# Optimization experiments

Measured on AMD Instinct MI355X. Metric: run time of the kernel, lower is better.

The kernel has to match this reference:

```python
import jax, jax.numpy as jnp
import numpy as np

B, L, D = 8, 2048, 1024
MASKED = -2.0 ** 31  # fp32 path of the torch code


def setup_inputs() -> dict:
    key = jax.random.key(0)
    ks = jax.random.split(key, 11)
    s = 1.0 / np.sqrt(D)
    return {
        "Q": jax.random.normal(ks[0], (B, L, D), jnp.float32),
        "K": jax.random.normal(ks[1], (B, L, D), jnp.float32),
        "V": jax.random.normal(ks[2], (B, L, D), jnp.float32),
        "Wq": jax.random.normal(ks[3], (D, D), jnp.float32) * s,
        "bq": jax.random.normal(ks[4], (D,), jnp.float32) * s,
        "Wk": jax.random.normal(ks[5], (D, D), jnp.float32) * s,
        "bk": jax.random.normal(ks[6], (D,), jnp.float32) * s,
        "Wv": jax.random.normal(ks[7], (D, D), jnp.float32) * s,
        "bv": jax.random.normal(ks[8], (D,), jnp.float32) * s,
        "q_mask": jax.random.randint(ks[9], (B, L), 0, 2, jnp.int32),
        "k_mask": jax.random.randint(ks[10], (B, L), 0, 2, jnp.int32),
    }


def reference(Q, K, V, Wq, bq, Wk, bk, Wv, bv, q_mask, k_mask):
    # with_projection=True: linear projections (torch Linear: x @ W.T + b)
    Qp = jnp.einsum("bld,ed->ble", Q, Wq) + bq
    Kp = jnp.einsum("bld,ed->ble", K, Wk) + bk
    Vp = jnp.einsum("bld,ed->ble", V, Wv) + bv
    # NOTE: source hard-sets scale = 1 after computing sqrt(d_hidden)
    e = jnp.einsum("bqd,bkd->bqk", Qp, Kp)            # [B, Lq, Lk]
    e = jnp.where(k_mask[:, None, :] == 0, MASKED, e)  # masked_fill on key axis
    a = jax.nn.softmax(e, axis=-1)                     # with_sparse=False
    # dropout is identity in eval/reference mode
    a = jnp.einsum("bqk,bkd->bqd", a, Vp)
    a = jnp.where(q_mask[:, :, None] == 0, 0.0, a)     # zero masked query rows
    return a, e
```

## Files before the change

### kernel.cpp

```cpp
#include <hip/hip_runtime.h>
#include <cstddef>
#include <cstdint>

constexpr int Bn = 8;
constexpr int Ln = 2048;
constexpr int Dn = 1024;
constexpr float MASKED_VAL = -2147483648.0f;

typedef unsigned short u16;
typedef unsigned int   u32;
typedef __attribute__((ext_vector_type(8))) __bf16 bf16x8;
typedef __attribute__((ext_vector_type(4))) float  f32x4;

__device__ __forceinline__ u16 f2bf(float x) {
    u32 u = __float_as_uint(x);
    u += 0x7FFFu + ((u >> 16) & 1u);
    return (u16)(u >> 16);
}
__device__ __forceinline__ float bf2f(u16 h) {
    return __uint_as_float(((u32)h) << 16);
}
__device__ __forceinline__ u32 pack2(float a, float b) {
    return (u32)f2bf(a) | ((u32)f2bf(b) << 16);
}
__device__ __forceinline__ int rup(int x, int m) { return (x + m - 1) & ~(m - 1); }

__device__ __forceinline__ void gload16(const void* g, void* l) {
    typedef const __attribute__((address_space(1))) unsigned int* gp_t;
    typedef __attribute__((address_space(3))) unsigned int* lp_t;
    __builtin_amdgcn_global_load_lds((gp_t)g, (lp_t)l, 16, 0, 0);
}

#define MFMA16(a, b, c) __builtin_amdgcn_mfma_f32_16x16x32_bf16((a), (b), (c), 0, 0, 0)

__global__ __launch_bounds__(256) void prep_kernel(
    const int* __restrict__ k_mask, const int* __restrict__ q_mask,
    int* __restrict__ kidx, int* __restrict__ kpos,
    int* __restrict__ qidx, int* __restrict__ qpos, int* __restrict__ cnts)
{
    __shared__ int sc[256];
    __shared__ int lastv;
    const int b = blockIdx.x, t = threadIdx.x;
    for (int pass = 0; pass < 2; ++pass) {
        const int* msk = (pass ? q_mask : k_mask) + b * Ln;
        int* idx = (pass ? qidx : kidx) + b * Ln;
        int* pos = (pass ? qpos : kpos) + b * Ln;
        int f[8], s = 0;
        #pragma unroll
        for (int j = 0; j < 8; ++j) { f[j] = (msk[t * 8 + j] != 0) ? 1 : 0; s += f[j]; }
        sc[t] = s;
        __syncthreads();
        #pragma unroll
        for (int o = 1; o < 256; o <<= 1) {
            int v = (t >= o) ? sc[t - o] : 0;
            __syncthreads();
            sc[t] += v;
            __syncthreads();
        }
        int incl = sc[t];
        int total = sc[255];
        int p = incl - s;
        #pragma unroll
        for (int j = 0; j < 8; ++j) {
            pos[t * 8 + j] = f[j] ? p : -1;
            if (f[j]) { idx[p] = t * 8 + j; ++p; }
        }
        __syncthreads();
        if (t == 0) {
            cnts[b * 2 + pass] = total;
            lastv = (total > 0) ? idx[total - 1] : 0;
        }
        __syncthreads();
        int padv = (pass == 0) ? lastv : 0;
        for (int e2 = total + t; e2 < Ln; e2 += 256) idx[e2] = padv;
        __syncthreads();
    }
}

__global__ __launch_bounds__(256) void convert_single_kernel(
    const float* __restrict__ src, u16* __restrict__ dh, int n)
{
    int i = (blockIdx.x * 256 + threadIdx.x) * 8;
    if (i >= n) return;
    float f[8];
    *(float4*)&f[0] = *(const float4*)(src + i);
    *(float4*)&f[4] = *(const float4*)(src + i + 4);
    u32 H[4];
    #pragma unroll
    for (int j = 0; j < 4; ++j) H[j] = pack2(f[2*j], f[2*j+1]);
    *(uint4*)(dh + i) = make_uint4(H[0], H[1], H[2], H[3]);
}

__global__ __launch_bounds__(256) void convgather_kernel(
    const float* __restrict__ K, const float* __restrict__ V,
    const int* __restrict__ kidx, const int* __restrict__ cnts,
    u16* __restrict__ Xkc, u16* __restrict__ Vc)
{
    const int b = blockIdx.z, j = blockIdx.x, y = blockIdx.y;
    if (j >= rup(cnts[b * 2], 128)) return;
    const int src_row = kidx[b * Ln + j];
    const float* src = (y ? V : K) + ((size_t)b * Ln + src_row) * Dn;
    u16* dst = (y ? Vc : Xkc) + ((size_t)b * Ln + j) * Dn;
    const int t = threadIdx.x;
    float4 f = *(const float4*)(src + t * 4);
    *(uint2*)(dst + t * 4) = make_uint2(pack2(f.x, f.y), pack2(f.z, f.w));
}

__global__ __launch_bounds__(256) void wtrans_kernel(
    const float* __restrict__ Wq, const float* __restrict__ Wk,
    u16* __restrict__ Wqt, u16* __restrict__ Wkt)
{
    __shared__ float tile[64][68];
    const float* src = blockIdx.z ? Wk : Wq;
    u16* dst = blockIdx.z ? Wkt : Wqt;
    const int e0 = blockIdx.y * 64, d0 = blockIdx.x * 64;
    const int t = threadIdx.x;
    const int r = t >> 2, cq = (t & 3) * 16;
    const float* s = src + (size_t)(e0 + r) * Dn + d0 + cq;
    #pragma unroll
    for (int i = 0; i < 4; ++i)
        *(float4*)&tile[r][cq + i * 4] = *(const float4*)(s + i * 4);
    __syncthreads();
    u32 o[8];
    #pragma unroll
    for (int i = 0; i < 8; ++i)
        o[i] = pack2(tile[cq + 2 * i][r], tile[cq + 2 * i + 1][r]);
    u16* d = dst + (size_t)(d0 + r) * Dn + e0 + cq;
    *(uint4*)(d)     = make_uint4(o[0], o[1], o[2], o[3]);
    *(uint4*)(d + 8) = make_uint4(o[4], o[5], o[6], o[7]);
}

__global__ __launch_bounds__(64) void ck_kernel(
    const float* __restrict__ bq, const float* __restrict__ bk, float* __restrict__ cbuf)
{
    int l = threadIdx.x;
    float s = 0.f;
    #pragma unroll
    for (int i = 0; i < 16; ++i) s += bq[l + 64 * i] * bk[l + 64 * i];
    #pragma unroll
    for (int o = 32; o; o >>= 1) s += __shfl_xor(s, o, 64);
    if (l == 0) cbuf[0] = s;
}

__global__ __launch_bounds__(256) void wvec_kernel(
    const u16* __restrict__ Wqt, const u16* __restrict__ Wkt,
    const float* __restrict__ bk, const float* __restrict__ bq,
    float* __restrict__ w1, float* __restrict__ w2)
{
    const int y = blockIdx.y;
    const u16* src = y ? Wkt : Wqt;
    const float* vec = y ? bq : bk;
    float* out = y ? w2 : w1;
    const int d = blockIdx.x * 4 + (threadIdx.x >> 6);
    const int l = threadIdx.x & 63;
    float s = 0.f;
    #pragma unroll
    for (int i = 0; i < 16; ++i) {
        int e = l + 64 * i;
        s += bf2f(src[(size_t)d * Dn + e]) * vec[e];
    }
    #pragma unroll
    for (int o = 32; o; o >>= 1) s += __shfl_xor(s, o, 64);
    if (l == 0) out[d] = s;
}

__global__ __launch_bounds__(256) void rowdot_kernel(
    const u16* __restrict__ Xq, const u16* __restrict__ Xkc,
    const float* __restrict__ w1, const float* __restrict__ w2,
    const float* __restrict__ cbuf, float* __restrict__ u, float* __restrict__ vc)
{
    const int y = blockIdx.y;
    const u16* x = y ? Xkc : Xq;
    const float* w = y ? w2 : w1;
    float* out = y ? vc : u;
    const int row = blockIdx.x * 4 + (threadIdx.x >> 6);
    const int l = threadIdx.x & 63;
    float s = 0.f;
    #pragma unroll
    for (int h = 0; h < 2; ++h) {
        const u16* xp = x + (size_t)row * Dn + h * 512 + l * 8;
        const float* wp = w + h * 512 + l * 8;
        uint4 xv = *(const uint4*)xp;
        float4 wa = *(const float4*)(wp);
        float4 wb = *(const float4*)(wp + 4);
        const u16* xs = (const u16*)&xv;
        s += bf2f(xs[0]) * wa.x + bf2f(xs[1]) * wa.y + bf2f(xs[2]) * wa.z + bf2f(xs[3]) * wa.w
           + bf2f(xs[4]) * wb.x + bf2f(xs[5]) * wb.y + bf2f(xs[6]) * wb.z + bf2f(xs[7]) * wb.w;
    }
    #pragma unroll
    for (int o = 32; o; o >>= 1) s += __shfl_xor(s, o, 64);
    if (l == 0) out[row] = s + (y ? 0.0f : cbuf[0]);
}

__global__ __launch_bounds__(256) void zeroa_kernel(
    float4* __restrict__ out_a, const int* __restrict__ q_mask)
{
    const int row = blockIdx.x;
    if (q_mask[row]) return;
    out_a[(size_t)row * 256 + threadIdx.x] = make_float4(0.f, 0.f, 0.f, 0.f);
}

__global__ __launch_bounds__(256) void mgemm_kernel(
    const u16* __restrict__ A, const u16* __restrict__ B, u16* __restrict__ C)
{
    __shared__ __align__(16) unsigned char As[128 * 128];
    __shared__ __align__(16) unsigned char Bs[128 * 128];

    const int m0 = blockIdx.y * 128, n0 = blockIdx.x * 128;
    const int tid = threadIdx.x, lane = tid & 63, wid = tid >> 6;
    const int wm = (wid >> 1) * 64, wn = (wid & 1) * 64;

    const u16* gA[4]; const u16* gB[4]; int ldsOff[4];
    #pragma unroll
    for (int q = 0; q < 4; ++q) {
        int c = wid * 4 + q;
        int row = c * 8 + (lane >> 3);
        int sig = (lane & 7) ^ (row & 7);
        gA[q] = A + (size_t)(m0 + row) * Dn + sig * 8;
        gB[q] = B + (size_t)(n0 + row) * Dn + sig * 8;
        ldsOff[q] = c * 1024;
    }

    f32x4 acc[4][4];
    const f32x4 z4 = {0.f, 0.f, 0.f, 0.f};
    #pragma unroll
    for (int i = 0; i < 4; ++i)
        #pragma unroll
        for (int j = 0; j < 4; ++j) acc[i][j] = z4;

    for (int k0 = 0; k0 < Dn; k0 += 64) {
        #pragma unroll
        for (int q = 0; q < 4; ++q) {
            gload16(gA[q], As + ldsOff[q]);
            gload16(gB[q], Bs + ldsOff[q]);
            gA[q] += 64; gB[q] += 64;
        }
        __syncthreads();

        const int sh = lane >> 4;
        #pragma unroll
        for (int s = 0; s < 2; ++s) {
            bf16x8 af[4], bf[4];
            #pragma unroll
            for (int i = 0; i < 4; ++i) {
                int row = wm + i * 16 + (lane & 15);
                af[i] = *(const bf16x8*)(As + row * 128 + (((s * 4 + sh) ^ (row & 7)) << 4));
            }
            #pragma unroll
            for (int j = 0; j < 4; ++j) {
                int row = wn + j * 16 + (lane & 15);
                bf[j] = *(const bf16x8*)(Bs + row * 128 + (((s * 4 + sh) ^ (row & 7)) << 4));
            }
            #pragma unroll
            for (int i = 0; i < 4; ++i)
                #pragma unroll
                for (int j = 0; j < 4; ++j)
                    acc[i][j] = MFMA16(af[i], bf[j], acc[i][j]);
        }
        __syncthreads();
    }

    #pragma unroll
    for (int i = 0; i < 4; ++i) {
        #pragma unroll
        for (int r = 0; r < 4; ++r) {
            int m = m0 + wm + i * 16 + (lane >> 4) * 4 + r;
            u16* oh = C + (size_t)m * Dn + n0 + wn;
            #pragma unroll
            for (int j = 0; j < 4; ++j)
                oh[j * 16 + (lane & 15)] = f2bf(acc[i][j][r]);
        }
    }
}

__global__ __launch_bounds__(256) void gt_kernel(
    const u16* __restrict__ Xkc, const u16* __restrict__ Mb,
    const int* __restrict__ cnts, u16* __restrict__ Gt)
{
    __shared__ __align__(16) unsigned char As[128 * 128];
    __shared__ __align__(16) unsigned char Bs[128 * 128];

    const int b = blockIdx.z;
    const int kc_b = cnts[b * 2];
    const int m0 = blockIdx.y * 128;
    if (m0 >= rup(kc_b, 128)) return;
    const int n0 = blockIdx.x * 128;
    const int tid = threadIdx.x, lane = tid & 63, wid = tid >> 6;
    const int wm = (wid >> 1) * 64, wn = (wid & 1) * 64;

    const u16* Xkc_b = Xkc + (size_t)b * Ln * Dn;

    const u16* gA[4]; const u16* gB[4]; int ldsOff[4];
    #pragma unroll
    for (int q = 0; q < 4; ++q) {
        int c = wid * 4 + q;
        int row = c * 8 + (lane >> 3);
        int sig = (lane & 7) ^ (row & 7);
        gA[q] = Xkc_b + (size_t)(m0 + row) * Dn + sig * 8;
        gB[q] = Mb + (size_t)(n0 + row) * Dn + sig * 8;
        ldsOff[q] = c * 1024;
    }

    f32x4 acc[4][4];
    const f32x4 z4 = {0.f, 0.f, 0.f, 0.f};
    #pragma unroll
    for (int i = 0; i < 4; ++i)
        #pragma unroll
        for (int j = 0; j < 4; ++j) acc[i][j] = z4;

    for (int k0 = 0; k0 < Dn; k0 += 64) {
        #pragma unroll
        for (int q = 0; q < 4; ++q) {
            gload16(gA[q], As + ldsOff[q]);
            gload16(gB[q], Bs + ldsOff[q]);
            gA[q] += 64; gB[q] += 64;
        }
        __syncthreads();

        const int sh = lane >> 4;
        #pragma unroll
        for (int s = 0; s < 2; ++s) {
            bf16x8 af[4], bf[4];
            #pragma unroll
            for (int i = 0; i < 4; ++i) {
                int row = wm + i * 16 + (lane & 15);
                af[i] = *(const bf16x8*)(As + row * 128 + (((s * 4 + sh) ^ (row & 7)) << 4));
            }
            #pragma unroll
            for (int j = 0; j < 4; ++j) {
                int row = wn + j * 16 + (lane & 15);
                bf[j] = *(const bf16x8*)(Bs + row * 128 + (((s * 4 + sh) ^ (row & 7)) << 4));
            }
            #pragma unroll
            for (int i = 0; i < 4; ++i)
                #pragma unroll
                for (int j = 0; j < 4; ++j)
                    acc[i][j] = MFMA16(af[i], bf[j], acc[i][j]);
        }
        __syncthreads();
    }

    u16* Gt_b = Gt + (size_t)b * Ln * Dn;
    #pragma unroll
    for (int i = 0; i < 4; ++i) {
        #pragma unroll
        for (int r = 0; r < 4; ++r) {
            int m = m0 + wm + i * 16 + (lane >> 4) * 4 + r;
            u16* oh = Gt_b + (size_t)m * Dn + n0 + wn;
            #pragma unroll
            for (int j = 0; j < 4; ++j)
                oh[j * 16 + (lane & 15)] = f2bf(acc[i][j][r]);
        }
    }
}

__global__ __launch_bounds__(256) void projv_kernel(
    const u16* __restrict__ Vc, const u16* __restrict__ Wvb,
    const float* __restrict__ bv, const int* __restrict__ cnts,
    u16* __restrict__ Vhc)
{
    __shared__ __align__(16) unsigned char As[128 * 128];
    __shared__ __align__(16) unsigned char Bs[128 * 128];

    const int b = blockIdx.z;
    const int kc_b = cnts[b * 2];
    const int m0 = blockIdx.y * 128;
    if (m0 >= rup(kc_b, 128)) return;
    const int n0 = blockIdx.x * 128;
    const int tid = threadIdx.x, lane = tid & 63, wid = tid >> 6;
    const int wm = (wid >> 1) * 64, wn = (wid & 1) * 64;

    const u16* Vc_b = Vc + (size_t)b * Ln * Dn;

    const u16* gA[4]; const u16* gB[4]; int ldsOff[4];
    #pragma unroll
    for (int q = 0; q < 4; ++q) {
        int c = wid * 4 + q;
        int row = c * 8 + (lane >> 3);
        int sig = (lane & 7) ^ (row & 7);
        gA[q] = Vc_b + (size_t)(m0 + row) * Dn + sig * 8;
        gB[q] = Wvb + (size_t)(n0 + row) * Dn + sig * 8;
        ldsOff[q] = c * 1024;
    }

    f32x4 acc[4][4];
    const f32x4 z4 = {0.f, 0.f, 0.f, 0.f};
    #pragma unroll
    for (int i = 0; i < 4; ++i)
        #pragma unroll
        for (int j = 0; j < 4; ++j) acc[i][j] = z4;

    for (int k0 = 0; k0 < Dn; k0 += 64) {
        #pragma unroll
        for (int q = 0; q < 4; ++q) {
            gload16(gA[q], As + ldsOff[q]);
            gload16(gB[q], Bs + ldsOff[q]);
            gA[q] += 64; gB[q] += 64;
        }
        __syncthreads();

        const int sh = lane >> 4;
        #pragma unroll
        for (int s = 0; s < 2; ++s) {
            bf16x8 af[4], bf[4];
            #pragma unroll
            for (int i = 0; i < 4; ++i) {
                int row = wm + i * 16 + (lane & 15);
                af[i] = *(const bf16x8*)(As + row * 128 + (((s * 4 + sh) ^ (row & 7)) << 4));
            }
            #pragma unroll
            for (int j = 0; j < 4; ++j) {
                int row = wn + j * 16 + (lane & 15);
                bf[j] = *(const bf16x8*)(Bs + row * 128 + (((s * 4 + sh) ^ (row & 7)) << 4));
            }
            #pragma unroll
            for (int i = 0; i < 4; ++i)
                #pragma unroll
                for (int j = 0; j < 4; ++j)
                    acc[i][j] = MFMA16(af[i], bf[j], acc[i][j]);
        }
        __syncthreads();
    }

    float bv4[4];
    #pragma unroll
    for (int j = 0; j < 4; ++j) bv4[j] = bv[n0 + wn + j * 16 + (lane & 15)];
    u16* Vhc_b = Vhc + (size_t)b * Ln * Dn;
    #pragma unroll
    for (int i = 0; i < 4; ++i) {
        #pragma unroll
        for (int r = 0; r < 4; ++r) {
            int m = m0 + wm + i * 16 + (lane >> 4) * 4 + r;
            u16* oh = Vhc_b + (size_t)m * Dn + n0 + wn;
            #pragma unroll
            for (int j = 0; j < 4; ++j)
                oh[j * 16 + (lane & 15)] = f2bf(acc[i][j][r] + bv4[j]);
        }
    }
}

__global__ __launch_bounds__(256) void vtransc_kernel(
    const u16* __restrict__ Vhc, const int* __restrict__ cnts,
    u16* __restrict__ Vtc)
{
    __shared__ u16 tile[64][72];
    const int b = blockIdx.z;
    const int l0 = blockIdx.y * 64, d0 = blockIdx.x * 64;
    if (l0 >= rup(cnts[b * 2], 64)) return;
    const int t = threadIdx.x;
    const int r = t >> 2, cq = (t & 3) * 16;

    const u16* src = Vhc + (size_t)(b * Ln + l0 + r) * Dn + d0 + cq;
    *(uint4*)&tile[r][cq]     = *(const uint4*)(src);
    *(uint4*)&tile[r][cq + 8] = *(const uint4*)(src + 8);
    __syncthreads();

    u16 tmp[16];
    #pragma unroll
    for (int i = 0; i < 16; ++i) tmp[i] = tile[cq + i][r];
    u16* dst = Vtc + (size_t)b * Dn * Ln + (size_t)(d0 + r) * Ln + l0 + cq;
    *(uint4*)(dst)     = *(uint4*)&tmp[0];
    *(uint4*)(dst + 8) = *(uint4*)&tmp[8];
}

__global__ __launch_bounds__(256) void scorec_kernel(
    const u16* __restrict__ Xq, const u16* __restrict__ Gt,
    const int* __restrict__ cnts,
    const float* __restrict__ u, const float* __restrict__ vc,
    u16* __restrict__ Ec)
{
    __shared__ __align__(16) unsigned char As[128 * 128];
    __shared__ __align__(16) unsigned char Bs[128 * 128];

    const int d = blockIdx.x;
    const int f = (d & 7) * 256 + (d >> 3);
    const int b = f >> 8;
    const int rem = f & 255;
    const int m0 = (rem >> 4) * 128;
    const int n0 = (rem & 15) * 128;

    const int kc_b = cnts[b * 2];
    if (n0 >= kc_b) return;
    const int tid = threadIdx.x, lane = tid & 63, wid = tid >> 6;
    const int wm = (wid >> 1) * 64, wn = (wid & 1) * 64;

    const size_t boff = (size_t)b * Ln * Dn;
    const u16* Xq_b = Xq + boff;
    const u16* Gt_b = Gt + boff;

    const u16* gA[4]; const u16* gB[4]; int ldsOff[4];
    #pragma unroll
    for (int q = 0; q < 4; ++q) {
        int c = wid * 4 + q;
        int row = c * 8 + (lane >> 3);
        int sig = (lane & 7) ^ (row & 7);
        gA[q] = Xq_b + (size_t)(m0 + row) * Dn + sig * 8;
        gB[q] = Gt_b + (size_t)(n0 + row) * Dn + sig * 8;
        ldsOff[q] = c * 1024;
    }

    f32x4 acc[4][4];
    const f32x4 z4 = {0.f, 0.f, 0.f, 0.f};
    #pragma unroll
    for (int i = 0; i < 4; ++i)
        #pragma unroll
        for (int j = 0; j < 4; ++j) acc[i][j] = z4;

    for (int k0 = 0; k0 < Dn; k0 += 64) {
        #pragma unroll
        for (int q = 0; q < 4; ++q) {
            gload16(gA[q], As + ldsOff[q]);
            gload16(gB[q], Bs + ldsOff[q]);
            gA[q] += 64; gB[q] += 64;
        }
        __syncthreads();

        const int sh = lane >> 4;
        #pragma unroll
        for (int s = 0; s < 2; ++s) {
            bf16x8 af[4], bf[4];
            #pragma unroll
            for (int i = 0; i < 4; ++i) {
                int row = wm + i * 16 + (lane & 15);
                af[i] = *(const bf16x8*)(As + row * 128 + (((s * 4 + sh) ^ (row & 7)) << 4));
            }
            #pragma unroll
            for (int j = 0; j < 4; ++j) {
                int row = wn + j * 16 + (lane & 15);
                bf[j] = *(const bf16x8*)(Bs + row * 128 + (((s * 4 + sh) ^ (row & 7)) << 4));
            }
            #pragma unroll
            for (int i = 0; i < 4; ++i)
                #pragma unroll
                for (int j = 0; j < 4; ++j)
                    acc[i][j] = MFMA16(af[i], bf[j], acc[i][j]);
        }
        __syncthreads();
    }

    float vcl[4];
    #pragma unroll
    for (int j = 0; j < 4; ++j) vcl[j] = vc[b * Ln + n0 + wn + j * 16 + (lane & 15)];
    #pragma unroll
    for (int i = 0; i < 4; ++i) {
        #pragma unroll
        for (int r = 0; r < 4; ++r) {
            int m = m0 + wm + i * 16 + (lane >> 4) * 4 + r;
            float um = u[b * Ln + m];
            u16* orow = Ec + ((size_t)(b * Ln + m)) * Ln + n0 + wn;
            #pragma unroll
            for (int j = 0; j < 4; ++j) {
                int jj = n0 + wn + j * 16 + (lane & 15);
                orow[j * 16 + (lane & 15)] =
                    f2bf((jj < kc_b) ? (acc[i][j][r] + um + vcl[j]) : MASKED_VAL);
            }
        }
    }
}

__global__ __launch_bounds__(256) void stats_expand_kernel(
    const u16* __restrict__ Ec, const int* __restrict__ kpos,
    const int* __restrict__ qpos, const int* __restrict__ cnts,
    u16* __restrict__ Pc, float* __restrict__ e)
{
    __shared__ float redm[4];
    __shared__ float reds[4];
    const int row = blockIdx.x;
    const int b = row >> 11;
    const int t = threadIdx.x;
    const u16* er = Ec + (size_t)row * Ln;
    const int qp = qpos[row];

    if (qp >= 0) {
        const int bound = rup(cnts[b * 2], 64);
        const int lane = t & 63, wave = t >> 6;
        float v[8];
        int base = t * 8;
        if (base < bound) {
            uint4 x = *(const uint4*)(er + base);
            const u16* xs = (const u16*)&x;
            #pragma unroll
            for (int j = 0; j < 8; ++j) v[j] = bf2f(xs[j]);
        } else {
            #pragma unroll
            for (int j = 0; j < 8; ++j) v[j] = MASKED_VAL;
        }

        float mx = v[0];
        #pragma unroll
        for (int j = 1; j < 8; ++j) mx = fmaxf(mx, v[j]);
        #pragma unroll
        for (int o = 32; o > 0; o >>= 1) mx = fmaxf(mx, __shfl_xor(mx, o, 64));
        if (lane == 0) redm[wave] = mx;
        __syncthreads();
        mx = fmaxf(fmaxf(redm[0], redm[1]), fmaxf(redm[2], redm[3]));

        float s = 0.f;
        #pragma unroll
        for (int j = 0; j < 8; ++j) s += __expf(v[j] - mx);
        #pragma unroll
        for (int o = 32; o > 0; o >>= 1) s += __shfl_xor(s, o, 64);
        if (lane == 0) reds[wave] = s;
        __syncthreads();
        s = reds[0] + reds[1] + reds[2] + reds[3];
        float sinv = 1.0f / s;

        u32 P[4];
        #pragma unroll
        for (int j = 0; j < 4; ++j)
            P[j] = pack2(__expf(v[2*j] - mx) * sinv, __expf(v[2*j+1] - mx) * sinv);
        u16* pr = Pc + ((size_t)b * Ln + qp) * Ln + t * 8;
        *(uint4*)pr = make_uint4(P[0], P[1], P[2], P[3]);
    }

    const int* kp = kpos + b * Ln;
    const int k = t * 8;
    int p[8];
    *(int4*)&p[0] = *(const int4*)(kp + k);
    *(int4*)&p[4] = *(const int4*)(kp + k + 4);
    float o[8];
    #pragma unroll
    for (int j = 0; j < 8; ++j)
        o[j] = (p[j] >= 0) ? bf2f(er[p[j]]) : MASKED_VAL;

    float* eo = e + (size_t)row * Ln + k;
    *(float4*)(eo)     = make_float4(o[0], o[1], o[2], o[3]);
    *(float4*)(eo + 4) = make_float4(o[4], o[5], o[6], o[7]);
}

__global__ __launch_bounds__(256) void pvc_kernel(
    const u16* __restrict__ Pc, const u16* __restrict__ Vtc,
    const int* __restrict__ qidx, const int* __restrict__ cnts,
    float* __restrict__ out_a)
{
    __shared__ __align__(16) unsigned char As[128 * 128];
    __shared__ __align__(16) unsigned char Bs[128 * 128];

    const int d = blockIdx.x;
    const int f = (d & 7) * 128 + (d >> 3);
    const int b = f >> 7;
    const int rem = f & 127;
    const int m0 = (rem >> 3) * 128;
    const int n0 = (rem & 7) * 128;

    const int kc_b = cnts[b * 2], qc_b = cnts[b * 2 + 1];
    if (m0 >= rup(qc_b, 128)) return;
    const int kbound = rup(kc_b, 64);
    const int tid = threadIdx.x, lane = tid & 63, wid = tid >> 6;
    const int wm = (wid >> 1) * 64, wn = (wid & 1) * 64;

    const u16* Pc_b  = Pc  + (size_t)b * Ln * Ln;
    const u16* Vtc_b = Vtc + (size_t)b * Dn * Ln;
    const int* qidx_b = qidx + b * Ln;

    const u16* gA[4]; const u16* gB[4]; int ldsOff[4];
    #pragma unroll
    for (int q = 0; q < 4; ++q) {
        int c = wid * 4 + q;
        int row = c * 8 + (lane >> 3);
        int sig = (lane & 7) ^ (row & 7);
        gA[q] = Pc_b  + (size_t)(m0 + row) * Ln + sig * 8;
        gB[q] = Vtc_b + (size_t)(n0 + row) * Ln + sig * 8;
        ldsOff[q] = c * 1024;
    }

    f32x4 acc[4][4];
    const f32x4 z4 = {0.f, 0.f, 0.f, 0.f};
    #pragma unroll
    for (int i = 0; i < 4; ++i)
        #pragma unroll
        for (int j = 0; j < 4; ++j) acc[i][j] = z4;

    for (int k0 = 0; k0 < kbound; k0 += 64) {
        #pragma unroll
        for (int q = 0; q < 4; ++q) {
            gload16(gA[q], As + ldsOff[q]);
            gload16(gB[q], Bs + ldsOff[q]);
            gA[q] += 64; gB[q] += 64;
        }
        __syncthreads();

        const int sh = lane >> 4;
        #pragma unroll
        for (int s = 0; s < 2; ++s) {
            bf16x8 af[4], bv[4];
            #pragma unroll
            for (int i = 0; i < 4; ++i) {
                int row = wm + i * 16 + (lane & 15);
                af[i] = *(const bf16x8*)(As + row * 128 + (((s * 4 + sh) ^ (row & 7)) << 4));
            }
            #pragma unroll
            for (int j = 0; j < 4; ++j) {
                int row = wn + j * 16 + (lane & 15);
                bv[j] = *(const bf16x8*)(Bs + row * 128 + (((s * 4 + sh) ^ (row & 7)) << 4));
            }
            #pragma unroll
            for (int i = 0; i < 4; ++i)
                #pragma unroll
                for (int j = 0; j < 4; ++j)
                    acc[i][j] = MFMA16(af[i], bv[j], acc[i][j]);
        }
        __syncthreads();
    }

    #pragma unroll
    for (int i = 0; i < 4; ++i) {
        #pragma unroll
        for (int r = 0; r < 4; ++r) {
            int gi = m0 + wm + i * 16 + (lane >> 4) * 4 + r;
            if (gi < qc_b) {
                int gm = qidx_b[gi];
                float* orow = out_a + (size_t)(b * Ln + gm) * Dn + n0 + wn;
                #pragma unroll
                for (int j = 0; j < 4; ++j)
                    orow[j * 16 + (lane & 15)] = acc[i][j][r];
            }
        }
    }
}

extern "C" void kernel_launch(void* const* d_in, const int* in_sizes, int n_in,
                              void* d_out, int out_size, void* d_ws, size_t ws_size,
                              hipStream_t stream)
{
    const float* Q  = (const float*)d_in[0];
    const float* K  = (const float*)d_in[1];
    const float* V  = (const float*)d_in[2];
    const float* Wq = (const float*)d_in[3];
    const float* bq = (const float*)d_in[4];
    const float* Wk = (const float*)d_in[5];
    const float* bk = (const float*)d_in[6];
    const float* Wv = (const float*)d_in[7];
    const float* bv = (const float*)d_in[8];
    const int* q_mask = (const int*)d_in[9];
    const int* k_mask = (const int*)d_in[10];

    float* out_a = (float*)d_out;
    float* out_e = out_a + (size_t)Bn * Ln * Dn;

    const size_t NE = (size_t)Bn * Ln * Dn;
    const size_t NW = (size_t)Dn * Dn;
    const int BL = Bn * Ln;

    u16* Vc  = (u16*)d_ws;
    u16* Xkc = Vc + NE;
    u16* Gt  = Xkc + NE;
    u16* Vhc = Gt + NE;
    u16* Xq  = Vhc + NE;
    u16* Vtc = Xq + NE;
    u16* Wvb = Vtc + NE;
    u16* Wqt = Wvb + NW;
    u16* Wkt = Wqt + NW;
    u16* Mb  = Wkt + NW;
    float* w1    = (float*)(Mb + NW);
    float* w2    = w1 + Dn;
    float* cbuf  = w2 + Dn;
    float* uarr  = cbuf + 4;
    float* vc    = uarr + BL;
    int* kidx = (int*)(vc + BL);
    int* kpos = kidx + BL;
    int* qidx = kpos + BL;
    int* qpos = qidx + BL;
    int* cnts = qpos + BL;

    u16* Ec = Vc;
    u16* Pc = Gt;

    dim3 blk(256);

    prep_kernel<<<dim3(Bn), blk, 0, stream>>>(k_mask, q_mask, kidx, kpos, qidx, qpos, cnts);

    convert_single_kernel<<<dim3(NE / 2048), blk, 0, stream>>>(Q, Xq, (int)NE);
    convgather_kernel<<<dim3(Ln, 2, Bn), blk, 0, stream>>>(K, V, kidx, cnts, Xkc, Vc);
    convert_single_kernel<<<dim3(NW / 2048), blk, 0, stream>>>(Wv, Wvb, (int)NW);

    wtrans_kernel<<<dim3(16, 16, 2), blk, 0, stream>>>(Wq, Wk, Wqt, Wkt);
    ck_kernel<<<dim3(1), dim3(64), 0, stream>>>(bq, bk, cbuf);
    wvec_kernel<<<dim3(256, 2), blk, 0, stream>>>(Wqt, Wkt, bk, bq, w1, w2);

    mgemm_kernel<<<dim3(8, 8), blk, 0, stream>>>(Wqt, Wkt, Mb);

    gt_kernel<<<dim3(Dn / 128, Ln / 128, Bn), blk, 0, stream>>>(Xkc, Mb, cnts, Gt);
    projv_kernel<<<dim3(Dn / 128, Ln / 128, Bn), blk, 0, stream>>>(
        Vc, Wvb, bv, cnts, Vhc);

    rowdot_kernel<<<dim3(BL / 4, 2), blk, 0, stream>>>(Xq, Xkc, w1, w2, cbuf, uarr, vc);

    vtransc_kernel<<<dim3(Dn / 64, Ln / 64, Bn), blk, 0, stream>>>(Vhc, cnts, Vtc);

    scorec_kernel<<<dim3(2048), blk, 0, stream>>>(Xq, Gt, cnts, uarr, vc, Ec);

    stats_expand_kernel<<<dim3(BL), blk, 0, stream>>>(Ec, kpos, qpos, cnts, Pc, out_e);

    zeroa_kernel<<<dim3(BL), blk, 0, stream>>>((float4*)out_a, q_mask);
    pvc_kernel<<<dim3(1024), blk, 0, stream>>>(Pc, Vtc, qidx, cnts, out_a);
}
```

Measured before the change: 339.8 us.

## Fuse weight prep, bias-vector dots, and zero-fill into fewer kernels

Merges the Wq/Wk transpose, Wv conversion, bias-weight vector products and bias constant into one wprep launch. The row dot products u and vc are computed inside the Q and K conversion kernels, so the separate rowdot pass that re-read the bf16 rows is gone. Zeroing of masked query rows moves into stats_expand, which drops the zeroa launch. This cuts launch count and memory re-reads, but the new w1/w2 computation is a serial loop over 1024 columns in only 8 blocks, which may sit on the critical path.

```diff
diff --git a/kernel.cpp b/kernel.cpp
--- a/kernel.cpp
+++ b/kernel.cpp
@@ -77,127 +77,110 @@
     }
 }
 
-__global__ __launch_bounds__(256) void convert_single_kernel(
-    const float* __restrict__ src, u16* __restrict__ dh, int n)
-{
-    int i = (blockIdx.x * 256 + threadIdx.x) * 8;
-    if (i >= n) return;
-    float f[8];
-    *(float4*)&f[0] = *(const float4*)(src + i);
-    *(float4*)&f[4] = *(const float4*)(src + i + 4);
-    u32 H[4];
-    #pragma unroll
-    for (int j = 0; j < 4; ++j) H[j] = pack2(f[2*j], f[2*j+1]);
-    *(uint4*)(dh + i) = make_uint4(H[0], H[1], H[2], H[3]);
-}
-
-__global__ __launch_bounds__(256) void convgather_kernel(
+__global__ __launch_bounds__(256) void wprep_kernel(
+    const float* __restrict__ Wq, const float* __restrict__ Wk, const float* __restrict__ Wv,
+    const float* __restrict__ bq, const float* __restrict__ bk,
+    u16* __restrict__ Wqt, u16* __restrict__ Wkt, u16* __restrict__ Wvb,
+    float* __restrict__ w1, float* __restrict__ w2, float* __restrict__ cbuf)
+{
+    __shared__ float tile[64][68];
+    const int blk = blockIdx.x;
+    const int t = threadIdx.x;
+
+    if (blk < 512) {
+        const float* src = (blk >= 256) ? Wk : Wq;
+        u16* dst = (blk >= 256) ? Wkt : Wqt;
+        const int rem = blk & 255;
+        const int e0 = (rem >> 4) * 64, d0 = (rem & 15) * 64;
+        const int r = t >> 2, cq = (t & 3) * 16;
+        const float* s = src + (size_t)(e0 + r) * Dn + d0 + cq;
+        #pragma unroll
+        for (int i = 0; i < 4; ++i)
+            *(float4*)&tile[r][cq + i * 4] = *(const float4*)(s + i * 4);
+        __syncthreads();
+        u32 o[8];
+        #pragma unroll
+        for (int i = 0; i < 8; ++i)
+            o[i] = pack2(tile[cq + 2 * i][r], tile[cq + 2 * i + 1][r]);
+        u16* d = dst + (size_t)(d0 + r) * Dn + e0 + cq;
+        *(uint4*)(d)     = make_uint4(o[0], o[1], o[2], o[3]);
+        *(uint4*)(d + 8) = make_uint4(o[4], o[5], o[6], o[7]);
+    } else if (blk < 1024) {
+        int i = ((blk - 512) * 256 + t) * 8;
+        float f[8];
+        *(float4*)&f[0] = *(const float4*)(Wv + i);
+        *(float4*)&f[4] = *(const float4*)(Wv + i + 4);
+        u32 H[4];
+        #pragma unroll
+        for (int j = 0; j < 4; ++j) H[j] = pack2(f[2*j], f[2*j+1]);
+        *(uint4*)(Wvb + i) = make_uint4(H[0], H[1], H[2], H[3]);
+    } else if (blk < 1032) {
+        const int rel = blk - 1024;
+        const float* W = (rel >> 2) ? Wk : Wq;
+        const float* vec = (rel >> 2) ? bq : bk;
+        float* out = (rel >> 2) ? w2 : w1;
+        const int dd = (rel & 3) * 256 + t;
+        float s = 0.f;
+        for (int e = 0; e < Dn; ++e) s += W[(size_t)e * Dn + dd] * vec[e];
+        out[dd] = s;
+    } else {
+        if (t < 64) {
+            float s = 0.f;
+            #pragma unroll
+            for (int i = 0; i < 16; ++i) s += bq[t + 64 * i] * bk[t + 64 * i];
+            #pragma unroll
+            for (int o = 32; o; o >>= 1) s += __shfl_xor(s, o, 64);
+            if (t == 0) cbuf[0] = s;
+        }
+    }
+}
+
+__global__ __launch_bounds__(256) void convq_kernel(
+    const float* __restrict__ Q, const float* __restrict__ w1,
+    const float* __restrict__ cbuf, u16* __restrict__ Xq, float* __restrict__ u)
+{
+    __shared__ float red[4];
+    const int row = blockIdx.x;
+    const int t = threadIdx.x;
+    float4 f = *(const float4*)(Q + (size_t)row * Dn + t * 4);
+    u32 p0 = pack2(f.x, f.y), p1 = pack2(f.z, f.w);
+    *(uint2*)(Xq + (size_t)row * Dn + t * 4) = make_uint2(p0, p1);
+
+    float4 w = *(const float4*)(w1 + t * 4);
+    float s = bf2f((u16)(p0 & 0xFFFFu)) * w.x + bf2f((u16)(p0 >> 16)) * w.y
+            + bf2f((u16)(p1 & 0xFFFFu)) * w.z + bf2f((u16)(p1 >> 16)) * w.w;
+    #pragma unroll
+    for (int o = 32; o; o >>= 1) s += __shfl_xor(s, o, 64);
+    if ((t & 63) == 0) red[t >> 6] = s;
+    __syncthreads();
+    if (t == 0) u[row] = red[0] + red[1] + red[2] + red[3] + cbuf[0];
+}
+
+__global__ __launch_bounds__(256) void convkv_kernel(
     const float* __restrict__ K, const float* __restrict__ V,
     const int* __restrict__ kidx, const int* __restrict__ cnts,
-    u16* __restrict__ Xkc, u16* __restrict__ Vc)
-{
+    const float* __restrict__ w2, u16* __restrict__ Xkc, u16* __restrict__ Vc,
+    float* __restrict__ vc)
+{
+    __shared__ float red[4];
     const int b = blockIdx.z, j = blockIdx.x, y = blockIdx.y;
     if (j >= rup(cnts[b * 2], 128)) return;
-    const int src_row = kidx[b * Ln + j];
-    const float* src = (y ? V : K) + ((size_t)b * Ln + src_row) * Dn;
-    u16* dst = (y ? Vc : Xkc) + ((size_t)b * Ln + j) * Dn;
+    const int srow = kidx[b * Ln + j];
     const int t = threadIdx.x;
-    float4 f = *(const float4*)(src + t * 4);
-    *(uint2*)(dst + t * 4) = make_uint2(pack2(f.x, f.y), pack2(f.z, f.w));
-}
-
-__global__ __launch_bounds__(256) void wtrans_kernel(
-    const float* __restrict__ Wq, const float* __restrict__ Wk,
-    u16* __restrict__ Wqt, u16* __restrict__ Wkt)
-{
-    __shared__ float tile[64][68];
-    const float* src = blockIdx.z ? Wk : Wq;
-    u16* dst = blockIdx.z ? Wkt : Wqt;
-    const int e0 = blockIdx.y * 64, d0 = blockIdx.x * 64;
-    const int t = threadIdx.x;
-    const int r = t >> 2, cq = (t & 3) * 16;
-    const float* s = src + (size_t)(e0 + r) * Dn + d0 + cq;
-    #pragma unroll
-    for (int i = 0; i < 4; ++i)
-        *(float4*)&tile[r][cq + i * 4] = *(const float4*)(s + i * 4);
-    __syncthreads();
-    u32 o[8];
-    #pragma unroll
-    for (int i = 0; i < 8; ++i)
-        o[i] = pack2(tile[cq + 2 * i][r], tile[cq + 2 * i + 1][r]);
-    u16* d = dst + (size_t)(d0 + r) * Dn + e0 + cq;
-    *(uint4*)(d)     = make_uint4(o[0], o[1], o[2], o[3]);
-    *(uint4*)(d + 8) = make_uint4(o[4], o[5], o[6], o[7]);
-}
-
-__global__ __launch_bounds__(64) void ck_kernel(
-    const float* __restrict__ bq, const float* __restrict__ bk, float* __restrict__ cbuf)
-{
-    int l = threadIdx.x;
-    float s = 0.f;
-    #pragma unroll
-    for (int i = 0; i < 16; ++i) s += bq[l + 64 * i] * bk[l + 64 * i];
-    #pragma unroll
-    for (int o = 32; o; o >>= 1) s += __shfl_xor(s, o, 64);
-    if (l == 0) cbuf[0] = s;
-}
-
-__global__ __launch_bounds__(256) void wvec_kernel(
-    const u16* __restrict__ Wqt, const u16* __restrict__ Wkt,
-    const float* __restrict__ bk, const float* __restrict__ bq,
-    float* __restrict__ w1, float* __restrict__ w2)
-{
-    const int y = blockIdx.y;
-    const u16* src = y ? Wkt : Wqt;
-    const float* vec = y ? bq : bk;
-    float* out = y ? w2 : w1;
-    const int d = blockIdx.x * 4 + (threadIdx.x >> 6);
-    const int l = threadIdx.x & 63;
-    float s = 0.f;
-    #pragma unroll
-    for (int i = 0; i < 16; ++i) {
-        int e = l + 64 * i;
-        s += bf2f(src[(size_t)d * Dn + e]) * vec[e];
-    }
-    #pragma unroll
-    for (int o = 32; o; o >>= 1) s += __shfl_xor(s, o, 64);
-    if (l == 0) out[d] = s;
-}
-
-__global__ __launch_bounds__(256) void rowdot_kernel(
-    const u16* __restrict__ Xq, const u16* __restrict__ Xkc,
-    const float* __restrict__ w1, const float* __restrict__ w2,
-    const float* __restrict__ cbuf, float* __restrict__ u, float* __restrict__ vc)
-{
-    const int y = blockIdx.y;
-    const u16* x = y ? Xkc : Xq;
-    const float* w = y ? w2 : w1;
-    float* out = y ? vc : u;
-    const int row = blockIdx.x * 4 + (threadIdx.x >> 6);
-    const int l = threadIdx.x & 63;
-    float s = 0.f;
-    #pragma unroll
-    for (int h = 0; h < 2; ++h) {
-        const u16* xp = x + (size_t)row * Dn + h * 512 + l * 8;
-        const float* wp = w + h * 512 + l * 8;
-        uint4 xv = *(const uint4*)xp;
-        float4 wa = *(const float4*)(wp);
-        float4 wb = *(const float4*)(wp + 4);
-        const u16* xs = (const u16*)&xv;
-        s += bf2f(xs[0]) * wa.x + bf2f(xs[1]) * wa.y + bf2f(xs[2]) * wa.z + bf2f(xs[3]) * wa.w
-           + bf2f(xs[4]) * wb.x + bf2f(xs[5]) * wb.y + bf2f(xs[6]) * wb.z + bf2f(xs[7]) * wb.w;
-    }
-    #pragma unroll
-    for (int o = 32; o; o >>= 1) s += __shfl_xor(s, o, 64);
-    if (l == 0) out[row] = s + (y ? 0.0f : cbuf[0]);
-}
-
-__global__ __launch_bounds__(256) void zeroa_kernel(
-    float4* __restrict__ out_a, const int* __restrict__ q_mask)
-{
-    const int row = blockIdx.x;
-    if (q_mask[row]) return;
-    out_a[(size_t)row * 256 + threadIdx.x] = make_float4(0.f, 0.f, 0.f, 0.f);
+    float4 f = *(const float4*)((y ? V : K) + ((size_t)b * Ln + srow) * Dn + t * 4);
+    u32 p0 = pack2(f.x, f.y), p1 = pack2(f.z, f.w);
+    *(uint2*)((y ? Vc : Xkc) + ((size_t)b * Ln + j) * Dn + t * 4) = make_uint2(p0, p1);
+
+    if (y == 0) {
+        float4 w = *(const float4*)(w2 + t * 4);
+        float s = bf2f((u16)(p0 & 0xFFFFu)) * w.x + bf2f((u16)(p0 >> 16)) * w.y
+                + bf2f((u16)(p1 & 0xFFFFu)) * w.z + bf2f((u16)(p1 >> 16)) * w.w;
+        #pragma unroll
+        for (int o = 32; o; o >>= 1) s += __shfl_xor(s, o, 64);
+        if ((t & 63) == 0) red[t >> 6] = s;
+        __syncthreads();
+        if (t == 0) vc[b * Ln + j] = red[0] + red[1] + red[2] + red[3];
+    }
 }
 
 __global__ __launch_bounds__(256) void mgemm_kernel(
@@ -561,7 +544,7 @@
 __global__ __launch_bounds__(256) void stats_expand_kernel(
     const u16* __restrict__ Ec, const int* __restrict__ kpos,
     const int* __restrict__ qpos, const int* __restrict__ cnts,
-    u16* __restrict__ Pc, float* __restrict__ e)
+    u16* __restrict__ Pc, float* __restrict__ e, float* __restrict__ out_a)
 {
     __shared__ float redm[4];
     __shared__ float reds[4];
@@ -611,6 +594,8 @@
             P[j] = pack2(__expf(v[2*j] - mx) * sinv, __expf(v[2*j+1] - mx) * sinv);
         u16* pr = Pc + ((size_t)b * Ln + qp) * Ln + t * 8;
         *(uint4*)pr = make_uint4(P[0], P[1], P[2], P[3]);
+    } else {
+        *(float4*)(out_a + (size_t)row * Dn + t * 4) = make_float4(0.f, 0.f, 0.f, 0.f);
     }
 
     const int* kp = kpos + b * Ln;
@@ -770,13 +755,12 @@
 
     prep_kernel<<<dim3(Bn), blk, 0, stream>>>(k_mask, q_mask, kidx, kpos, qidx, qpos, cnts);
 
-    convert_single_kernel<<<dim3(NE / 2048), blk, 0, stream>>>(Q, Xq, (int)NE);
-    convgather_kernel<<<dim3(Ln, 2, Bn), blk, 0, stream>>>(K, V, kidx, cnts, Xkc, Vc);
-    convert_single_kernel<<<dim3(NW / 2048), blk, 0, stream>>>(Wv, Wvb, (int)NW);
-
-    wtrans_kernel<<<dim3(16, 16, 2), blk, 0, stream>>>(Wq, Wk, Wqt, Wkt);
-    ck_kernel<<<dim3(1), dim3(64), 0, stream>>>(bq, bk, cbuf);
-    wvec_kernel<<<dim3(256, 2), blk, 0, stream>>>(Wqt, Wkt, bk, bq, w1, w2);
+    wprep_kernel<<<dim3(1033), blk, 0, stream>>>(
+        Wq, Wk, Wv, bq, bk, Wqt, Wkt, Wvb, w1, w2, cbuf);
+
+    convq_kernel<<<dim3(BL), blk, 0, stream>>>(Q, w1, cbuf, Xq, uarr);
+    convkv_kernel<<<dim3(Ln, 2, Bn), blk, 0, stream>>>(
+        K, V, kidx, cnts, w2, Xkc, Vc, vc);
 
     mgemm_kernel<<<dim3(8, 8), blk, 0, stream>>>(Wqt, Wkt, Mb);
 
@@ -784,14 +768,12 @@
     projv_kernel<<<dim3(Dn / 128, Ln / 128, Bn), blk, 0, stream>>>(
         Vc, Wvb, bv, cnts, Vhc);
 
-    rowdot_kernel<<<dim3(BL / 4, 2), blk, 0, stream>>>(Xq, Xkc, w1, w2, cbuf, uarr, vc);
-
     vtransc_kernel<<<dim3(Dn / 64, Ln / 64, Bn), blk, 0, stream>>>(Vhc, cnts, Vtc);
 
     scorec_kernel<<<dim3(2048), blk, 0, stream>>>(Xq, Gt, cnts, uarr, vc, Ec);
 
-    stats_expand_kernel<<<dim3(BL), blk, 0, stream>>>(Ec, kpos, qpos, cnts, Pc, out_e);
-
-    zeroa_kernel<<<dim3(BL), blk, 0, stream>>>((float4*)out_a, q_mask);
+    stats_expand_kernel<<<dim3(BL), blk, 0, stream>>>(
+        Ec, kpos, qpos, cnts, Pc, out_e, out_a);
+
     pvc_kernel<<<dim3(1024), blk, 0, stream>>>(Pc, Vtc, qidx, cnts, out_a);
 }
```

Result: slower. 367.4 us (+8.1%).
